# Kernel tuning notes

Hardware: AMD Instinct MI355X
Metric: run time of the kernel (lower is better)

The kernel has to match this reference:

```python
import jax, jax.numpy as jnp
import numpy as np

B, S, E, H = 4, 2048, 16, 4  # batch, seq, embed_dim (= n_wires), num_heads
D_K = E // H


def setup_inputs() -> dict:
    key = jax.random.key(0)
    k1, k2, k3, k4, k5 = jax.random.split(key, 5)
    return {
        "x": jax.random.normal(k1, (B, S, E), dtype=jnp.float32),
        "theta": jax.random.normal(k2, (E,), dtype=jnp.float32),
        "Wk": jax.random.normal(k3, (E, E), dtype=jnp.float32) / np.float32(np.sqrt(E)),
        "Wv": jax.random.normal(k4, (E, E), dtype=jnp.float32) / np.float32(np.sqrt(E)),
        "Wc": jax.random.normal(k5, (E, E), dtype=jnp.float32) / np.float32(np.sqrt(E)),
    }


def _split_heads(t):
    # [B, S, E] -> [B, H, S, D_K]
    b, s, _ = t.shape
    return t.reshape(b, s, H, D_K).transpose(0, 2, 1, 3)


def reference(x, theta, Wk, Wv, Wc):
    # Quantum head: RX(x_i) then RX(theta_i) on wire i from |0>, measure PauliZ.
    # Single-qubit RX rotations on disjoint wires factorize: <Z_i> = cos(x_i + theta_i).
    q = jnp.cos(x + theta)          # [B, S, E] (batched over all tokens at once)
    k = x @ Wk.T                    # nn.Linear(bias=False): x @ W^T
    v = x @ Wv.T

    qh, kh, vh = _split_heads(q), _split_heads(k), _split_heads(v)
    scale = np.float32(1.0 / np.sqrt(D_K))
    scores = jnp.einsum("bhqd,bhkd->bhqk", qh, kh) * scale  # [B, H, S, S]
    attn = jax.nn.softmax(scores, axis=-1)
    out = jnp.einsum("bhqk,bhkd->bhqd", attn, vh)           # [B, H, S, D_K]
    out = out.transpose(0, 2, 1, 3).reshape(x.shape)        # [B, S, E]
    return out @ Wc.T
```

## Files before the change

kernel.cpp:

```cpp
#include <hip/hip_runtime.h>
#include <math.h>

#define BB 4
#define SS 2048
#define EE 16
#define HH 4
#define DK 4
#define KS 16
#define NQ (BB*HH*SS)
#define KLEN (SS/KS)

#define QSCALE 0.7213475204444817f

__global__ __launch_bounds__(256) void proj_kernel(
    const float* __restrict__ x, const float* __restrict__ theta,
    const float* __restrict__ Wk, const float* __restrict__ Wv,
    float* __restrict__ qarr, float* __restrict__ kv)
{
    int t = blockIdx.x * 256 + threadIdx.x;
    int b = t >> 11;
    int s = t & (SS - 1);

    float xv[EE];
    const float4* xr = reinterpret_cast<const float4*>(x + t * EE);
    #pragma unroll
    for (int e4 = 0; e4 < 4; ++e4) {
        float4 v = xr[e4];
        xv[e4*4+0] = v.x; xv[e4*4+1] = v.y; xv[e4*4+2] = v.z; xv[e4*4+3] = v.w;
    }

    float qv[EE];
    #pragma unroll
    for (int e = 0; e < EE; ++e)
        qv[e] = __cosf(xv[e] + theta[e]) * QSCALE;

    float kd[EE], vd[EE];
    #pragma unroll
    for (int d = 0; d < EE; ++d) {
        float ak = 0.f, av = 0.f;
        #pragma unroll
        for (int e = 0; e < EE; ++e) {
            ak = fmaf(xv[e], Wk[d*EE + e], ak);
            av = fmaf(xv[e], Wv[d*EE + e], av);
        }
        kd[d] = ak; vd[d] = av;
    }

    #pragma unroll
    for (int h = 0; h < HH; ++h) {
        int gq = (b*HH + h)*SS + s;
        *reinterpret_cast<float4*>(qarr + (size_t)gq*4) =
            make_float4(qv[h*4+0], qv[h*4+1], qv[h*4+2], qv[h*4+3]);
        float4* kvp = reinterpret_cast<float4*>(kv + (size_t)gq*8);
        kvp[0] = make_float4(kd[h*4+0], kd[h*4+1], kd[h*4+2], kd[h*4+3]);
        kvp[1] = make_float4(vd[h*4+0], vd[h*4+1], vd[h*4+2], vd[h*4+3]);
    }
}

__global__ __launch_bounds__(256) void attn_kernel(
    const float* __restrict__ qarr, const float* __restrict__ kv,
    float* __restrict__ accp, float* __restrict__ lp)
{
    __shared__ float4 skv[KLEN * 2];

    int bh = blockIdx.z;
    int ks = blockIdx.y;
    int qp = blockIdx.x * 256 + threadIdx.x;
    int gq0 = bh * SS + qp * 2;

    const float4* kvp =
        reinterpret_cast<const float4*>(kv + ((size_t)bh*SS + (size_t)ks*KLEN)*8);
    skv[threadIdx.x] = kvp[threadIdx.x];

    const float4* qp4 = reinterpret_cast<const float4*>(qarr + (size_t)gq0*4);
    float4 q0 = qp4[0];
    float4 q1 = qp4[1];

    __syncthreads();

    float l0 = 0.f, l1 = 0.f;
    float a0x = 0.f, a0y = 0.f, a0z = 0.f, a0w = 0.f;
    float a1x = 0.f, a1y = 0.f, a1z = 0.f, a1w = 0.f;
    #pragma unroll 8
    for (int s = 0; s < KLEN; ++s) {
        float4 kk = skv[2*s];
        float4 vv = skv[2*s + 1];
        float sc0 = fmaf(q0.x, kk.x, fmaf(q0.y, kk.y, fmaf(q0.z, kk.z, q0.w*kk.w)));
        float sc1 = fmaf(q1.x, kk.x, fmaf(q1.y, kk.y, fmaf(q1.z, kk.z, q1.w*kk.w)));
        float p0 = __builtin_amdgcn_exp2f(sc0);
        float p1 = __builtin_amdgcn_exp2f(sc1);
        l0 += p0; l1 += p1;
        a0x = fmaf(p0, vv.x, a0x); a0y = fmaf(p0, vv.y, a0y);
        a0z = fmaf(p0, vv.z, a0z); a0w = fmaf(p0, vv.w, a0w);
        a1x = fmaf(p1, vv.x, a1x); a1y = fmaf(p1, vv.y, a1y);
        a1z = fmaf(p1, vv.z, a1z); a1w = fmaf(p1, vv.w, a1w);
    }

    float4* ap = reinterpret_cast<float4*>(accp + ((size_t)ks*NQ + gq0)*4);
    ap[0] = make_float4(a0x, a0y, a0z, a0w);
    ap[1] = make_float4(a1x, a1y, a1z, a1w);
    *reinterpret_cast<float2*>(lp + (size_t)ks*NQ + gq0) = make_float2(l0, l1);
}

__global__ __launch_bounds__(256) void out_kernel(
    const float* __restrict__ accp, const float* __restrict__ lp,
    const float* __restrict__ Wc, float* __restrict__ out)
{
    int t = blockIdx.x * 256 + threadIdx.x;
    int b = t >> 11;
    int s = t & (SS - 1);

    float attn[EE];
    #pragma unroll
    for (int h = 0; h < HH; ++h) {
        int gq = (b*HH + h)*SS + s;
        float ax = 0.f, ay = 0.f, az = 0.f, aw = 0.f, l = 0.f;
        #pragma unroll
        for (int ks = 0; ks < KS; ++ks) {
            float4 a = *reinterpret_cast<const float4*>(accp + ((size_t)ks*NQ + gq)*4);
            ax += a.x; ay += a.y; az += a.z; aw += a.w;
            l += lp[(size_t)ks*NQ + gq];
        }
        float inv = 1.0f / l;
        attn[h*4+0] = ax*inv; attn[h*4+1] = ay*inv;
        attn[h*4+2] = az*inv; attn[h*4+3] = aw*inv;
    }

    float4* orow = reinterpret_cast<float4*>(out + (size_t)t * EE);
    #pragma unroll
    for (int e4 = 0; e4 < 4; ++e4) {
        float o[4];
        #pragma unroll
        for (int i = 0; i < 4; ++i) {
            int e = e4*4 + i;
            float acc = 0.f;
            #pragma unroll
            for (int j = 0; j < EE; ++j)
                acc = fmaf(attn[j], Wc[e*EE + j], acc);
            o[i] = acc;
        }
        orow[e4] = make_float4(o[0], o[1], o[2], o[3]);
    }
}

extern "C" void kernel_launch(void* const* d_in, const int* in_sizes, int n_in,
                              void* d_out, int out_size, void* d_ws, size_t ws_size,
                              hipStream_t stream)
{
    const float* x     = (const float*)d_in[0];
    const float* theta = (const float*)d_in[1];
    const float* Wk    = (const float*)d_in[2];
    const float* Wv    = (const float*)d_in[3];
    const float* Wc    = (const float*)d_in[4];
    float* out = (float*)d_out;

    float* ws   = (float*)d_ws;
    float* qarr = ws;
    float* kvb  = qarr + (size_t)NQ*4;
    float* accp = kvb  + (size_t)NQ*8;
    float* lp   = accp + (size_t)KS*NQ*4;

    proj_kernel<<<dim3((BB*SS)/256), 256, 0, stream>>>(x, theta, Wk, Wv, qarr, kvb);
    attn_kernel<<<dim3(SS/(2*256), KS, BB*HH), 256, 0, stream>>>(qarr, kvb, accp, lp);
    out_kernel<<<dim3((BB*SS)/256), 256, 0, stream>>>(accp, lp, Wc, out);
}
```

Before: 98.43 us.

## Process eight queries per thread with packed float2 FMAs in attention

Each attention thread now handles eight queries instead of two, so each shared-memory K/V load is reused across more queries. The score and accumulation math uses two-wide vector types, which can map to packed FP32 FMA instructions. The key dimension is split into 32 chunks instead of 16 to keep enough blocks in flight, which doubles the partial-sum traffic that out_kernel must reduce. Register pressure per thread grows with the larger accumulator set.

```diff
diff --git a/kernel.cpp b/kernel.cpp
--- a/kernel.cpp
+++ b/kernel.cpp
@@ -6,11 +6,14 @@
 #define EE 16
 #define HH 4
 #define DK 4
-#define KS 16
+#define KS 32
 #define NQ (BB*HH*SS)
 #define KLEN (SS/KS)
+#define QPT 8
 
 #define QSCALE 0.7213475204444817f
+
+typedef float v2f __attribute__((ext_vector_type(2)));
 
 __global__ __launch_bounds__(256) void proj_kernel(
     const float* __restrict__ x, const float* __restrict__ theta,
@@ -63,43 +66,65 @@
 {
     __shared__ float4 skv[KLEN * 2];
 
-    int bh = blockIdx.z;
-    int ks = blockIdx.y;
-    int qp = blockIdx.x * 256 + threadIdx.x;
-    int gq0 = bh * SS + qp * 2;
+    int ks = blockIdx.x;
+    int bh = blockIdx.y;
+    int gq0 = bh * SS + threadIdx.x * QPT;
 
     const float4* kvp =
         reinterpret_cast<const float4*>(kv + ((size_t)bh*SS + (size_t)ks*KLEN)*8);
-    skv[threadIdx.x] = kvp[threadIdx.x];
+    if (threadIdx.x < KLEN * 2) skv[threadIdx.x] = kvp[threadIdx.x];
 
-    const float4* qp4 = reinterpret_cast<const float4*>(qarr + (size_t)gq0*4);
-    float4 q0 = qp4[0];
-    float4 q1 = qp4[1];
+    const float4* qv4 = reinterpret_cast<const float4*>(qarr + (size_t)gq0*4);
+    v2f qx[4], qy[4], qz[4], qw[4];
+    #pragma unroll
+    for (int j = 0; j < 4; ++j) {
+        float4 qa = qv4[2*j], qb = qv4[2*j+1];
+        qx[j] = (v2f){qa.x, qb.x};
+        qy[j] = (v2f){qa.y, qb.y};
+        qz[j] = (v2f){qa.z, qb.z};
+        qw[j] = (v2f){qa.w, qb.w};
+    }
 
     __syncthreads();
 
-    float l0 = 0.f, l1 = 0.f;
-    float a0x = 0.f, a0y = 0.f, a0z = 0.f, a0w = 0.f;
-    float a1x = 0.f, a1y = 0.f, a1z = 0.f, a1w = 0.f;
-    #pragma unroll 8
+    v2f accxy[QPT] = {}, acczw[QPT] = {};
+    v2f lsum[4] = {};
+
+    #pragma unroll 4
     for (int s = 0; s < KLEN; ++s) {
         float4 kk = skv[2*s];
         float4 vv = skv[2*s + 1];
-        float sc0 = fmaf(q0.x, kk.x, fmaf(q0.y, kk.y, fmaf(q0.z, kk.z, q0.w*kk.w)));
-        float sc1 = fmaf(q1.x, kk.x, fmaf(q1.y, kk.y, fmaf(q1.z, kk.z, q1.w*kk.w)));
-        float p0 = __builtin_amdgcn_exp2f(sc0);
-        float p1 = __builtin_amdgcn_exp2f(sc1);
-        l0 += p0; l1 += p1;
-        a0x = fmaf(p0, vv.x, a0x); a0y = fmaf(p0, vv.y, a0y);
-        a0z = fmaf(p0, vv.z, a0z); a0w = fmaf(p0, vv.w, a0w);
-        a1x = fmaf(p1, vv.x, a1x); a1y = fmaf(p1, vv.y, a1y);
-        a1z = fmaf(p1, vv.z, a1z); a1w = fmaf(p1, vv.w, a1w);
+        v2f kx = (v2f){kk.x, kk.x};
+        v2f ky = (v2f){kk.y, kk.y};
+        v2f kz = (v2f){kk.z, kk.z};
+        v2f kw = (v2f){kk.w, kk.w};
+        v2f vxy = (v2f){vv.x, vv.y};
+        v2f vzw = (v2f){vv.z, vv.w};
+        #pragma unroll
+        for (int j = 0; j < 4; ++j) {
+            v2f sc = __builtin_elementwise_fma(qx[j], kx,
+                     __builtin_elementwise_fma(qy[j], ky,
+                     __builtin_elementwise_fma(qz[j], kz, qw[j] * kw)));
+            v2f p;
+            p.x = __builtin_amdgcn_exp2f(sc.x);
+            p.y = __builtin_amdgcn_exp2f(sc.y);
+            lsum[j] += p;
+            v2f p0 = __builtin_shufflevector(p, p, 0, 0);
+            v2f p1 = __builtin_shufflevector(p, p, 1, 1);
+            accxy[2*j]   = __builtin_elementwise_fma(p0, vxy, accxy[2*j]);
+            acczw[2*j]   = __builtin_elementwise_fma(p0, vzw, acczw[2*j]);
+            accxy[2*j+1] = __builtin_elementwise_fma(p1, vxy, accxy[2*j+1]);
+            acczw[2*j+1] = __builtin_elementwise_fma(p1, vzw, acczw[2*j+1]);
+        }
     }
 
     float4* ap = reinterpret_cast<float4*>(accp + ((size_t)ks*NQ + gq0)*4);
-    ap[0] = make_float4(a0x, a0y, a0z, a0w);
-    ap[1] = make_float4(a1x, a1y, a1z, a1w);
-    *reinterpret_cast<float2*>(lp + (size_t)ks*NQ + gq0) = make_float2(l0, l1);
+    #pragma unroll
+    for (int i = 0; i < QPT; ++i)
+        ap[i] = make_float4(accxy[i].x, accxy[i].y, acczw[i].x, acczw[i].y);
+    #pragma unroll
+    for (int j = 0; j < 4; ++j)
+        *reinterpret_cast<v2f*>(lp + (size_t)ks*NQ + gq0 + 2*j) = lsum[j];
 }
 
 __global__ __launch_bounds__(256) void out_kernel(
@@ -161,6 +186,6 @@
     float* lp   = accp + (size_t)KS*NQ*4;
 
     proj_kernel<<<dim3((BB*SS)/256), 256, 0, stream>>>(x, theta, Wk, Wv, qarr, kvb);
-    attn_kernel<<<dim3(SS/(2*256), KS, BB*HH), 256, 0, stream>>>(qarr, kvb, accp, lp);
+    attn_kernel<<<dim3(KS, BB*HH), 256, 0, stream>>>(qarr, kvb, accp, lp);
     out_kernel<<<dim3((BB*SS)/256), 256, 0, stream>>>(accp, lp, Wc, out);
 }
```

New measurement: 105.5 us. +7.2%, slower.

## Fuse projection into attention kernel and compute K/V per key tile in-block

Applied to the files above, without the earlier changes.

Removes the separate projection kernel: each attention block loads its key-tile slice of x into shared memory, computes K/V for its head with a small subset of threads, and computes cosine queries directly from x. Each thread now handles four queries across the whole sequence, and the grid shrinks to one block per (key split, batch*head). The output kernel is relaunched with 64-thread blocks to increase block count. This saves a launch and the q/kv workspace round trip but leaves only 256 blocks of 512 threads and serializes K/V compute on 128 threads per block.

```diff
diff --git a/kernel.cpp b/kernel.cpp
--- a/kernel.cpp
+++ b/kernel.cpp
@@ -9,104 +9,98 @@
 #define KS 16
 #define NQ (BB*HH*SS)
 #define KLEN (SS/KS)
+#define QPT 4
 
 #define QSCALE 0.7213475204444817f
 
-__global__ __launch_bounds__(256) void proj_kernel(
+__global__ __launch_bounds__(512) void attn_fused(
     const float* __restrict__ x, const float* __restrict__ theta,
     const float* __restrict__ Wk, const float* __restrict__ Wv,
-    float* __restrict__ qarr, float* __restrict__ kv)
-{
-    int t = blockIdx.x * 256 + threadIdx.x;
-    int b = t >> 11;
-    int s = t & (SS - 1);
-
-    float xv[EE];
-    const float4* xr = reinterpret_cast<const float4*>(x + t * EE);
-    #pragma unroll
-    for (int e4 = 0; e4 < 4; ++e4) {
-        float4 v = xr[e4];
-        xv[e4*4+0] = v.x; xv[e4*4+1] = v.y; xv[e4*4+2] = v.z; xv[e4*4+3] = v.w;
-    }
-
-    float qv[EE];
-    #pragma unroll
-    for (int e = 0; e < EE; ++e)
-        qv[e] = __cosf(xv[e] + theta[e]) * QSCALE;
-
-    float kd[EE], vd[EE];
-    #pragma unroll
-    for (int d = 0; d < EE; ++d) {
-        float ak = 0.f, av = 0.f;
-        #pragma unroll
-        for (int e = 0; e < EE; ++e) {
-            ak = fmaf(xv[e], Wk[d*EE + e], ak);
-            av = fmaf(xv[e], Wv[d*EE + e], av);
-        }
-        kd[d] = ak; vd[d] = av;
-    }
-
-    #pragma unroll
-    for (int h = 0; h < HH; ++h) {
-        int gq = (b*HH + h)*SS + s;
-        *reinterpret_cast<float4*>(qarr + (size_t)gq*4) =
-            make_float4(qv[h*4+0], qv[h*4+1], qv[h*4+2], qv[h*4+3]);
-        float4* kvp = reinterpret_cast<float4*>(kv + (size_t)gq*8);
-        kvp[0] = make_float4(kd[h*4+0], kd[h*4+1], kd[h*4+2], kd[h*4+3]);
-        kvp[1] = make_float4(vd[h*4+0], vd[h*4+1], vd[h*4+2], vd[h*4+3]);
-    }
-}
-
-__global__ __launch_bounds__(256) void attn_kernel(
-    const float* __restrict__ qarr, const float* __restrict__ kv,
     float* __restrict__ accp, float* __restrict__ lp)
 {
+    __shared__ float  sx[KLEN * EE];
     __shared__ float4 skv[KLEN * 2];
 
-    int bh = blockIdx.z;
-    int ks = blockIdx.y;
-    int qp = blockIdx.x * 256 + threadIdx.x;
-    int gq0 = bh * SS + qp * 2;
+    int tid = threadIdx.x;
+    int ks = blockIdx.x;
+    int bh = blockIdx.y;
+    int b = bh >> 2;
+    int h = bh & 3;
 
-    const float4* kvp =
-        reinterpret_cast<const float4*>(kv + ((size_t)bh*SS + (size_t)ks*KLEN)*8);
-    skv[threadIdx.x] = kvp[threadIdx.x];
+    const float4* xsrc =
+        reinterpret_cast<const float4*>(x + ((size_t)b*SS + (size_t)ks*KLEN) * EE);
+    reinterpret_cast<float4*>(sx)[tid] = xsrc[tid];
 
-    const float4* qp4 = reinterpret_cast<const float4*>(qarr + (size_t)gq0*4);
-    float4 q0 = qp4[0];
-    float4 q1 = qp4[1];
+    float th0 = theta[h*4+0], th1 = theta[h*4+1];
+    float th2 = theta[h*4+2], th3 = theta[h*4+3];
+    float4 qv[QPT];
+    #pragma unroll
+    for (int j = 0; j < QPT; ++j) {
+        int s = tid + j*512;
+        float4 xq = *reinterpret_cast<const float4*>(
+            x + ((size_t)b*SS + s) * EE + h*4);
+        qv[j].x = __cosf(xq.x + th0) * QSCALE;
+        qv[j].y = __cosf(xq.y + th1) * QSCALE;
+        qv[j].z = __cosf(xq.z + th2) * QSCALE;
+        qv[j].w = __cosf(xq.w + th3) * QSCALE;
+    }
 
     __syncthreads();
 
-    float l0 = 0.f, l1 = 0.f;
-    float a0x = 0.f, a0y = 0.f, a0z = 0.f, a0w = 0.f;
-    float a1x = 0.f, a1y = 0.f, a1z = 0.f, a1w = 0.f;
+    if (tid < KLEN) {
+        const float4* xr = reinterpret_cast<const float4*>(sx + tid * EE);
+        float4 x0 = xr[0], x1 = xr[1], x2 = xr[2], x3 = xr[3];
+        float xv[EE] = {x0.x,x0.y,x0.z,x0.w, x1.x,x1.y,x1.z,x1.w,
+                        x2.x,x2.y,x2.z,x2.w, x3.x,x3.y,x3.z,x3.w};
+        float kd[DK], vd[DK];
+        #pragma unroll
+        for (int d = 0; d < DK; ++d) {
+            float ak = 0.f, av = 0.f;
+            #pragma unroll
+            for (int e = 0; e < EE; ++e) {
+                ak = fmaf(xv[e], Wk[(h*4+d)*EE + e], ak);
+                av = fmaf(xv[e], Wv[(h*4+d)*EE + e], av);
+            }
+            kd[d] = ak; vd[d] = av;
+        }
+        skv[2*tid]   = make_float4(kd[0], kd[1], kd[2], kd[3]);
+        skv[2*tid+1] = make_float4(vd[0], vd[1], vd[2], vd[3]);
+    }
+
+    __syncthreads();
+
+    float4 acc[QPT] = {};
+    float  lsum[QPT] = {};
     #pragma unroll 8
     for (int s = 0; s < KLEN; ++s) {
         float4 kk = skv[2*s];
         float4 vv = skv[2*s + 1];
-        float sc0 = fmaf(q0.x, kk.x, fmaf(q0.y, kk.y, fmaf(q0.z, kk.z, q0.w*kk.w)));
-        float sc1 = fmaf(q1.x, kk.x, fmaf(q1.y, kk.y, fmaf(q1.z, kk.z, q1.w*kk.w)));
-        float p0 = __builtin_amdgcn_exp2f(sc0);
-        float p1 = __builtin_amdgcn_exp2f(sc1);
-        l0 += p0; l1 += p1;
-        a0x = fmaf(p0, vv.x, a0x); a0y = fmaf(p0, vv.y, a0y);
-        a0z = fmaf(p0, vv.z, a0z); a0w = fmaf(p0, vv.w, a0w);
-        a1x = fmaf(p1, vv.x, a1x); a1y = fmaf(p1, vv.y, a1y);
-        a1z = fmaf(p1, vv.z, a1z); a1w = fmaf(p1, vv.w, a1w);
+        #pragma unroll
+        for (int j = 0; j < QPT; ++j) {
+            float sc = fmaf(qv[j].x, kk.x, fmaf(qv[j].y, kk.y,
+                       fmaf(qv[j].z, kk.z, qv[j].w * kk.w)));
+            float p = __builtin_amdgcn_exp2f(sc);
+            lsum[j] += p;
+            acc[j].x = fmaf(p, vv.x, acc[j].x);
+            acc[j].y = fmaf(p, vv.y, acc[j].y);
+            acc[j].z = fmaf(p, vv.z, acc[j].z);
+            acc[j].w = fmaf(p, vv.w, acc[j].w);
+        }
     }
 
-    float4* ap = reinterpret_cast<float4*>(accp + ((size_t)ks*NQ + gq0)*4);
-    ap[0] = make_float4(a0x, a0y, a0z, a0w);
-    ap[1] = make_float4(a1x, a1y, a1z, a1w);
-    *reinterpret_cast<float2*>(lp + (size_t)ks*NQ + gq0) = make_float2(l0, l1);
+    #pragma unroll
+    for (int j = 0; j < QPT; ++j) {
+        int gq = bh*SS + tid + j*512;
+        *reinterpret_cast<float4*>(accp + ((size_t)ks*NQ + gq)*4) = acc[j];
+        lp[(size_t)ks*NQ + gq] = lsum[j];
+    }
 }
 
-__global__ __launch_bounds__(256) void out_kernel(
+__global__ __launch_bounds__(64) void out_kernel(
     const float* __restrict__ accp, const float* __restrict__ lp,
     const float* __restrict__ Wc, float* __restrict__ out)
 {
-    int t = blockIdx.x * 256 + threadIdx.x;
+    int t = blockIdx.x * 64 + threadIdx.x;
     int b = t >> 11;
     int s = t & (SS - 1);
 
@@ -155,12 +149,9 @@
     float* out = (float*)d_out;
 
     float* ws   = (float*)d_ws;
-    float* qarr = ws;
-    float* kvb  = qarr + (size_t)NQ*4;
-    float* accp = kvb  + (size_t)NQ*8;
+    float* accp = ws;
     float* lp   = accp + (size_t)KS*NQ*4;
 
-    proj_kernel<<<dim3((BB*SS)/256), 256, 0, stream>>>(x, theta, Wk, Wv, qarr, kvb);
-    attn_kernel<<<dim3(SS/(2*256), KS, BB*HH), 256, 0, stream>>>(qarr, kvb, accp, lp);
-    out_kernel<<<dim3((BB*SS)/256), 256, 0, stream>>>(accp, lp, Wc, out);
+    attn_fused<<<dim3(KS, BB*HH), 512, 0, stream>>>(x, theta, Wk, Wv, accp, lp);
+    out_kernel<<<dim3((BB*SS)/64), 64, 0, stream>>>(accp, lp, Wc, out);
 }
```

Measured after the change: 92.48 us. 1.06x faster.
